# Performance work log

Hardware: AMD Instinct MI355X
Metric: run time of the kernel (lower is better)

Reference implementation:

```python
import jax, jax.numpy as jnp
import numpy as np

B, S, D, F, E, TOPK = 4, 2048, 1024, 4096, 8, 2


def setup_inputs() -> dict:
    key = jax.random.key(0)
    ks = jax.random.split(key, 8)
    sc = 0.02
    return {
        "x": jax.random.normal(ks[0], (B, S, D), dtype=jnp.float32),
        "Wg": jax.random.normal(ks[1], (D, E), dtype=jnp.float32) * sc,
        "bg": jnp.zeros((E,), dtype=jnp.float32),
        "W1": jax.random.normal(ks[2], (E, D, F), dtype=jnp.float32) * sc,
        "b1": jnp.zeros((E, F), dtype=jnp.float32),
        "W2": jax.random.normal(ks[3], (E, F, D), dtype=jnp.float32) * sc,
        "b2": jnp.zeros((E, D), dtype=jnp.float32),
    }


def reference(x, Wg, bg, W1, b1, W2, b2):
    # Router: top-k over gate logits, softmax over the k selected logits.
    logits = jnp.einsum("bsd,de->bse", x, Wg) + bg            # [B,S,E]
    top_vals, top_idx = jax.lax.top_k(logits, TOPK)            # [B,S,K]
    gates = jax.nn.softmax(top_vals, axis=-1)                  # [B,S,K]
    # Combine weights per expert: zero for unselected experts (same math
    # as the original masked gather/scatter loop). [B,S,E]
    comb = jnp.sum(jax.nn.one_hot(top_idx, E, dtype=x.dtype) * gates[..., None], axis=-2)
    xf = x.reshape(-1, D)                                      # [T,D], T=B*S
    cf = comb.reshape(-1, E)                                   # [T,E]
    # Expert FFNs (dropout is identity in eval): relu(x W1 + b1) W2 + b2
    h = jax.nn.relu(jnp.einsum("td,edf->etf", xf, W1) + b1[:, None, :])  # [E,T,F]
    y = jnp.einsum("etf,efd->etd", h, W2) + b2[:, None, :]               # [E,T,D]
    out = jnp.einsum("te,etd->td", cf, y)                                # [T,D]
    return out.reshape(B, S, D)
```

## Files before the change

### kernel.cpp

```cpp
#include <hip/hip_runtime.h>
#include <hip/hip_bf16.h>

#define T_TOK 8192
#define D_DIM 1024
#define F_DIM 4096
#define E_NUM 8
#define BM 128
#define MAX_ROWS (2 * T_TOK + E_NUM * BM)
#define NUM_RB (MAX_ROWS / BM)

typedef __hip_bfloat16 bf16;
using bf16x8  = __attribute__((ext_vector_type(8))) __bf16;
using float4v = __attribute__((ext_vector_type(4))) float;

__device__ inline void gl_lds16(const bf16* g, bf16* l) {
    __builtin_amdgcn_global_load_lds(
        (const __attribute__((address_space(1))) void*)g,
        (__attribute__((address_space(3))) void*)l, 16, 0, 0);
}

#define PH(WAITSTR, CA, CB, DOSTAGE, KST)                                      \
    do {                                                                       \
        asm volatile("s_waitcnt " WAITSTR ::: "memory");                       \
        __builtin_amdgcn_s_barrier();                                          \
        bf16x8 af[4], bfr[4];                                                  \
        _Pragma("unroll")                                                      \
        for (int m_ = 0; m_ < 4; ++m_)                                         \
            af[m_] = *(const bf16x8*)&(CA)[(wrow + m_ * 16 + fr) * 32 + fkk];  \
        _Pragma("unroll")                                                      \
        for (int n_ = 0; n_ < 4; ++n_)                                         \
            bfr[n_] = *(const bf16x8*)&(CB)[(wcol + n_ * 16 + fr) * 32 + fkk]; \
        asm volatile("s_waitcnt lgkmcnt(0)" ::: "memory");                     \
        __builtin_amdgcn_sched_barrier(0);                                     \
        __builtin_amdgcn_s_barrier();                                          \
        if (DOSTAGE) stage(KST, CA, CB);                                       \
        __builtin_amdgcn_s_setprio(1);                                         \
        _Pragma("unroll")                                                      \
        for (int m_ = 0; m_ < 4; ++m_)                                         \
            _Pragma("unroll")                                                  \
            for (int n_ = 0; n_ < 4; ++n_)                                     \
                acc[m_][n_] = __builtin_amdgcn_mfma_f32_16x16x32_bf16(         \
                    af[m_], bfr[n_], acc[m_][n_], 0, 0, 0);                    \
        __builtin_amdgcn_s_setprio(0);                                         \
    } while (0)

__global__ __launch_bounds__(256) void transpose_both(
    const float* __restrict__ W1, bf16* __restrict__ W1t,
    const float* __restrict__ W2, bf16* __restrict__ W2t) {
    __shared__ float tile[64][65];
    const int flat = blockIdx.x;
    const float* s;
    bf16* d;
    int M, N, n0, m0;
    if (flat < 8192) {
        const int e = flat >> 10, rem = flat & 1023;
        M = D_DIM; N = F_DIM;
        n0 = (rem & 63) * 64; m0 = (rem >> 6) * 64;
        s = W1 + (size_t)e * M * N;
        d = W1t + (size_t)e * M * N;
    } else {
        const int f2 = flat - 8192;
        const int e = f2 >> 10, rem = f2 & 1023;
        M = F_DIM; N = D_DIM;
        n0 = (rem & 15) * 64; m0 = (rem >> 4) * 64;
        s = W2 + (size_t)e * M * N;
        d = W2t + (size_t)e * M * N;
    }
    const int tx = threadIdx.x & 15, ty = threadIdx.x >> 4;
#pragma unroll
    for (int i = 0; i < 4; ++i) {
        const int r = ty + i * 16;
        const float4 v = *(const float4*)&s[(size_t)(m0 + r) * N + n0 + tx * 4];
        tile[r][tx * 4 + 0] = v.x;
        tile[r][tx * 4 + 1] = v.y;
        tile[r][tx * 4 + 2] = v.z;
        tile[r][tx * 4 + 3] = v.w;
    }
    __syncthreads();
#pragma unroll
    for (int i = 0; i < 4; ++i) {
        const int nc = ty + i * 16;
        bf16 o[4];
#pragma unroll
        for (int j = 0; j < 4; ++j) o[j] = __float2bfloat16(tile[tx * 4 + j][nc]);
        *(ushort4*)&d[(size_t)(n0 + nc) * M + m0 + tx * 4] = *(const ushort4*)o;
    }
}

__global__ __launch_bounds__(256) void router_xcvt_kernel(
    const float* __restrict__ x, const float* __restrict__ Wg,
    const float* __restrict__ bg, int* __restrict__ top_idx,
    float* __restrict__ top_gate, bf16* __restrict__ xb) {
    const int lane = threadIdx.x & 63;
    const int t = blockIdx.x * 4 + (threadIdx.x >> 6);
    const float* xrow = x + (size_t)t * D_DIM;

    float acc[E_NUM];
#pragma unroll
    for (int e = 0; e < E_NUM; ++e) acc[e] = 0.f;
#pragma unroll
    for (int it = 0; it < D_DIM / 64; ++it) {
        const int d = it * 64 + lane;
        const float xv = xrow[d];
        const float4 w0 = *(const float4*)&Wg[d * 8];
        const float4 w1 = *(const float4*)&Wg[d * 8 + 4];
        acc[0] += xv * w0.x; acc[1] += xv * w0.y;
        acc[2] += xv * w0.z; acc[3] += xv * w0.w;
        acc[4] += xv * w1.x; acc[5] += xv * w1.y;
        acc[6] += xv * w1.z; acc[7] += xv * w1.w;
    }
#pragma unroll
    for (int off = 32; off > 0; off >>= 1) {
#pragma unroll
        for (int e = 0; e < E_NUM; ++e) acc[e] += __shfl_xor(acc[e], off, 64);
    }
    if (lane == 0) {
        float v[E_NUM];
#pragma unroll
        for (int e = 0; e < E_NUM; ++e) v[e] = acc[e] + bg[e];
        int i0 = 0;
#pragma unroll
        for (int e = 1; e < E_NUM; ++e)
            if (v[e] > v[i0]) i0 = e;
        int i1 = -1;
#pragma unroll
        for (int e = 0; e < E_NUM; ++e) {
            if (e == i0) continue;
            if (i1 < 0 || v[e] > v[i1]) i1 = e;
        }
        const float g0 = 1.f / (1.f + expf(v[i1] - v[i0]));
        top_idx[2 * t] = i0;
        top_idx[2 * t + 1] = i1;
        top_gate[2 * t] = g0;
        top_gate[2 * t + 1] = 1.f - g0;
    }
    const float4* xs = (const float4*)(x + (size_t)blockIdx.x * 4 * D_DIM);
    ushort4* xd = (ushort4*)(xb + (size_t)blockIdx.x * 4 * D_DIM);
    for (int i = threadIdx.x; i < D_DIM; i += 256) {
        float4 v = xs[i];
        bf16 tmp[4];
        tmp[0] = __float2bfloat16(v.x);
        tmp[1] = __float2bfloat16(v.y);
        tmp[2] = __float2bfloat16(v.z);
        tmp[3] = __float2bfloat16(v.w);
        xd[i] = *(const ushort4*)tmp;
    }
}

__global__ __launch_bounds__(256) void count_offsets_kernel(
    const int* __restrict__ top_idx, int* __restrict__ offsets) {
    __shared__ int whist[4][E_NUM];
    int cnt[E_NUM];
#pragma unroll
    for (int e = 0; e < E_NUM; ++e) cnt[e] = 0;
    for (int i = threadIdx.x; i < 2 * T_TOK; i += 256) {
        const int idx = top_idx[i];
#pragma unroll
        for (int e = 0; e < E_NUM; ++e) cnt[e] += (idx == e) ? 1 : 0;
    }
#pragma unroll
    for (int off = 32; off > 0; off >>= 1) {
#pragma unroll
        for (int e = 0; e < E_NUM; ++e) cnt[e] += __shfl_xor(cnt[e], off, 64);
    }
    const int lane = threadIdx.x & 63, w = threadIdx.x >> 6;
    if (lane == 0) {
#pragma unroll
        for (int e = 0; e < E_NUM; ++e) whist[w][e] = cnt[e];
    }
    __syncthreads();
    if (threadIdx.x == 0) {
        int o = 0;
#pragma unroll
        for (int e = 0; e < E_NUM; ++e) {
            const int c = whist[0][e] + whist[1][e] + whist[2][e] + whist[3][e];
            offsets[e] = o;
            o += (c + BM - 1) / BM * BM;
        }
        offsets[E_NUM] = o;
    }
}

__global__ __launch_bounds__(256) void scatter_kernel(
    const int* __restrict__ top_idx, const float* __restrict__ top_gate,
    const int* __restrict__ offsets, int* __restrict__ cursors,
    int* __restrict__ tok_list, float* __restrict__ gate_list) {
    __shared__ int lhist[E_NUM];
    __shared__ int lbase[E_NUM];
    if (threadIdx.x < E_NUM) lhist[threadIdx.x] = 0;
    __syncthreads();

    const int t = blockIdx.x * 256 + threadIdx.x;
    int e0 = top_idx[2 * t], e1 = top_idx[2 * t + 1];
    int p0 = atomicAdd(&lhist[e0], 1);
    int p1 = atomicAdd(&lhist[e1], 1);
    __syncthreads();
    if (threadIdx.x < E_NUM)
        lbase[threadIdx.x] = atomicAdd(&cursors[threadIdx.x], lhist[threadIdx.x]);
    __syncthreads();

    const float g0 = top_gate[2 * t], g1 = top_gate[2 * t + 1];
    const int s0 = offsets[e0] + lbase[e0] + p0;
    const int s1 = offsets[e1] + lbase[e1] + p1;
    tok_list[s0] = t;
    gate_list[s0] = g0;
    tok_list[s1] = t;
    gate_list[s1] = g1;
}

__global__ __launch_bounds__(256, 4) void gemm1_kernel(
    const bf16* __restrict__ xb, const bf16* __restrict__ W1t,
    const float* __restrict__ b1, const int* __restrict__ tok_list,
    const int* __restrict__ offsets, bf16* __restrict__ hbuf) {
    __shared__ bf16 As0[BM * 32];
    __shared__ bf16 As1[BM * 32];
    __shared__ bf16 Bs0[BM * 32];
    __shared__ bf16 Bs1[BM * 32];
    __shared__ int toks[BM];

    const int NCB = F_DIM / 128;
    const int per = (NUM_RB * NCB) / 8;
    const int flat = blockIdx.x;
    const int sw = (flat & 7) * per + (flat >> 3);
    const int rb = sw / NCB, cb = sw % NCB;

    const int row0 = rb * BM;
    const int total = offsets[E_NUM];
    if (row0 >= total) return;
    int e = 0;
#pragma unroll
    for (int i = 1; i < E_NUM; ++i) e += (row0 >= offsets[i]) ? 1 : 0;

    const int tid = threadIdx.x;
    if (tid < BM) toks[tid] = tok_list[row0 + tid];
    __syncthreads();

    const int lane = tid & 63;
    const int w = tid >> 6;
    const int f0 = cb * 128;

    const int r0 = w * 16 + (lane >> 2);
    const int r1 = 64 + w * 16 + (lane >> 2);
    const int c16 = (lane & 3) ^ ((lane >> 3) & 3);
    int t0 = toks[r0]; if (t0 < 0) t0 = 0;
    int t1 = toks[r1]; if (t1 < 0) t1 = 0;
    const bf16* aP0 = xb + (size_t)t0 * D_DIM + c16 * 8;
    const bf16* aP1 = xb + (size_t)t1 * D_DIM + c16 * 8;
    const bf16* bP0 = W1t + ((size_t)e * F_DIM + f0 + r0) * D_DIM + c16 * 8;
    const bf16* bP1 = W1t + ((size_t)e * F_DIM + f0 + r1) * D_DIM + c16 * 8;

    const unsigned dO0 = __builtin_amdgcn_readfirstlane(w * 1024);
    const unsigned dO1 = __builtin_amdgcn_readfirstlane(4096 + w * 1024);

    const int wrow = (w >> 1) * 64, wcol = (w & 1) * 64;
    const int fr = lane & 15;
    const int fkk = 8 * ((lane >> 4) ^ ((lane >> 1) & 3));

    float4v acc[4][4];
#pragma unroll
    for (int m = 0; m < 4; ++m)
#pragma unroll
        for (int n = 0; n < 4; ++n)
#pragma unroll
            for (int r = 0; r < 4; ++r) acc[m][n][r] = 0.f;

    auto stage = [&](int kt, bf16* A, bf16* B) {
        const int ko = kt * 32;
        gl_lds16(aP0 + ko, (bf16*)((char*)A + dO0));
        gl_lds16(aP1 + ko, (bf16*)((char*)A + dO1));
        gl_lds16(bP0 + ko, (bf16*)((char*)B + dO0));
        gl_lds16(bP1 + ko, (bf16*)((char*)B + dO1));
    };

    const int NKT = D_DIM / 32;
    stage(0, As0, Bs0);
    stage(1, As1, Bs1);
    for (int kt = 0; kt < NKT - 2; kt += 2) {
        PH("vmcnt(4)", As0, Bs0, true, kt + 2);
        PH("vmcnt(4)", As1, Bs1, true, kt + 3);
    }
    PH("vmcnt(4)", As0, Bs0, false, 0);
    PH("vmcnt(0)", As1, Bs1, false, 0);

#pragma unroll
    for (int n = 0; n < 4; ++n) {
        const int gcol = f0 + wcol + n * 16 + fr;
        const float bias = b1[e * F_DIM + gcol];
#pragma unroll
        for (int m = 0; m < 4; ++m) {
#pragma unroll
            for (int r = 0; r < 4; ++r) {
                const int grow = row0 + wrow + m * 16 + (lane >> 4) * 4 + r;
                float v = acc[m][n][r] + bias;
                v = fmaxf(v, 0.f);
                hbuf[(size_t)grow * F_DIM + gcol] = __float2bfloat16(v);
            }
        }
    }
}

__global__ __launch_bounds__(256, 4) void gemm2_kernel(
    const bf16* __restrict__ hbuf, const bf16* __restrict__ W2t,
    const float* __restrict__ b2, const int* __restrict__ tok_list,
    const float* __restrict__ gate_list, const int* __restrict__ offsets,
    float* __restrict__ out) {
    __shared__ bf16 As0[BM * 32];
    __shared__ bf16 As1[BM * 32];
    __shared__ bf16 Bs0[BM * 32];
    __shared__ bf16 Bs1[BM * 32];
    __shared__ int toks[BM];
    __shared__ float gates_s[BM];

    const int NCB = D_DIM / 128;
    const int per = (NUM_RB * NCB) / 8;
    const int flat = blockIdx.x;
    const int sw = (flat & 7) * per + (flat >> 3);
    const int rb = sw / NCB, cb = sw % NCB;

    const int row0 = rb * BM;
    const int total = offsets[E_NUM];
    if (row0 >= total) return;
    int e = 0;
#pragma unroll
    for (int i = 1; i < E_NUM; ++i) e += (row0 >= offsets[i]) ? 1 : 0;

    const int tid = threadIdx.x;
    if (tid < BM) {
        int t = tok_list[row0 + tid];
        toks[tid] = t;
        gates_s[tid] = (t >= 0) ? gate_list[row0 + tid] : 0.f;
    }
    __syncthreads();

    const int lane = tid & 63;
    const int w = tid >> 6;
    const int d0 = cb * 128;

    const int r0 = w * 16 + (lane >> 2);
    const int r1 = 64 + w * 16 + (lane >> 2);
    const int c16 = (lane & 3) ^ ((lane >> 3) & 3);
    const bf16* aP0 = hbuf + (size_t)(row0 + r0) * F_DIM + c16 * 8;
    const bf16* aP1 = hbuf + (size_t)(row0 + r1) * F_DIM + c16 * 8;
    const bf16* bP0 = W2t + ((size_t)e * D_DIM + d0 + r0) * F_DIM + c16 * 8;
    const bf16* bP1 = W2t + ((size_t)e * D_DIM + d0 + r1) * F_DIM + c16 * 8;

    const unsigned dO0 = __builtin_amdgcn_readfirstlane(w * 1024);
    const unsigned dO1 = __builtin_amdgcn_readfirstlane(4096 + w * 1024);

    const int wrow = (w >> 1) * 64, wcol = (w & 1) * 64;
    const int fr = lane & 15;
    const int fkk = 8 * ((lane >> 4) ^ ((lane >> 1) & 3));

    float4v acc[4][4];
#pragma unroll
    for (int m = 0; m < 4; ++m)
#pragma unroll
        for (int n = 0; n < 4; ++n)
#pragma unroll
            for (int r = 0; r < 4; ++r) acc[m][n][r] = 0.f;

    auto stage = [&](int kt, bf16* A, bf16* B) {
        const int ko = kt * 32;
        gl_lds16(aP0 + ko, (bf16*)((char*)A + dO0));
        gl_lds16(aP1 + ko, (bf16*)((char*)A + dO1));
        gl_lds16(bP0 + ko, (bf16*)((char*)B + dO0));
        gl_lds16(bP1 + ko, (bf16*)((char*)B + dO1));
    };

    const int NKT = F_DIM / 32;
    stage(0, As0, Bs0);
    stage(1, As1, Bs1);
    for (int kt = 0; kt < NKT - 2; kt += 2) {
        PH("vmcnt(4)", As0, Bs0, true, kt + 2);
        PH("vmcnt(4)", As1, Bs1, true, kt + 3);
    }
    PH("vmcnt(4)", As0, Bs0, false, 0);
    PH("vmcnt(0)", As1, Bs1, false, 0);

#pragma unroll
    for (int n = 0; n < 4; ++n) {
        const int gcol = d0 + wcol + n * 16 + fr;
        const float bias = b2[e * D_DIM + gcol];
#pragma unroll
        for (int m = 0; m < 4; ++m) {
#pragma unroll
            for (int r = 0; r < 4; ++r) {
                const int lrow = wrow + m * 16 + (lane >> 4) * 4 + r;
                const int t = toks[lrow];
                if (t >= 0) {
                    const float v = (acc[m][n][r] + bias) * gates_s[lrow];
                    atomicAdd(&out[(size_t)t * D_DIM + gcol], v);
                }
            }
        }
    }
}

extern "C" void kernel_launch(void* const* d_in, const int* in_sizes, int n_in,
                              void* d_out, int out_size, void* d_ws, size_t ws_size,
                              hipStream_t stream) {
    const float* x = (const float*)d_in[0];
    const float* Wg = (const float*)d_in[1];
    const float* bg = (const float*)d_in[2];
    const float* W1 = (const float*)d_in[3];
    const float* b1 = (const float*)d_in[4];
    const float* W2 = (const float*)d_in[5];
    const float* b2 = (const float*)d_in[6];
    float* out = (float*)d_out;

    char* ws = (char*)d_ws;
    int* cursors = (int*)(ws + 32);
    int* offsets = (int*)(ws + 64);
    int* top_idx = (int*)(ws + 256);
    float* top_gate = (float*)(ws + 256 + 65536);
    int* tok_list = (int*)(ws + 256 + 2 * 65536);
    float* gate_list = (float*)(ws + 256 + 2 * 65536 + 69632);
    size_t off = 256 + 2 * 65536 + 2 * 69632;
    bf16* xb = (bf16*)(ws + off);
    off += (size_t)T_TOK * D_DIM * 2;
    bf16* W1t = (bf16*)(ws + off);
    off += (size_t)E_NUM * D_DIM * F_DIM * 2;
    bf16* W2t = (bf16*)(ws + off);
    off += (size_t)E_NUM * D_DIM * F_DIM * 2;
    bf16* hbuf = (bf16*)(ws + off);

    hipMemsetAsync(d_out, 0, (size_t)T_TOK * D_DIM * sizeof(float), stream);
    hipMemsetAsync(ws, 0, 64, stream);
    hipMemsetAsync(tok_list, 0xFF, (size_t)MAX_ROWS * 4, stream);

    transpose_both<<<16384, 256, 0, stream>>>(W1, W1t, W2, W2t);
    router_xcvt_kernel<<<T_TOK / 4, 256, 0, stream>>>(x, Wg, bg, top_idx, top_gate, xb);
    count_offsets_kernel<<<1, 256, 0, stream>>>(top_idx, offsets);
    scatter_kernel<<<T_TOK / 256, 256, 0, stream>>>(top_idx, top_gate, offsets, cursors,
                                                    tok_list, gate_list);
    gemm1_kernel<<<NUM_RB * (F_DIM / 128), 256, 0, stream>>>(xb, W1t, b1, tok_list,
                                                             offsets, hbuf);
    gemm2_kernel<<<NUM_RB * (D_DIM / 128), 256, 0, stream>>>(hbuf, W2t, b2, tok_list,
                                                             gate_list, offsets, out);
}
```

Baseline: 583.5 us.

## Replace atomic scatter with per-slot output buffer and reduction; fuse transposes into other kernels

gemm2 now writes gated expert outputs to a per-slot buffer instead of atomically adding into the output. A new reduce kernel sums each token's two slots using slot indices recorded by the scatter kernel, which also removes the output memset. The W1 transpose is merged into the router launch and the W2 transpose into the gemm1 launch as extra blocks, so they can overlap with other work. The change adds a large intermediate write and read, and reuses the xb/W1t workspace region for that buffer.

```diff
diff --git a/kernel.cpp b/kernel.cpp
--- a/kernel.cpp
+++ b/kernel.cpp
@@ -8,6 +8,7 @@
 #define BM 128
 #define MAX_ROWS (2 * T_TOK + E_NUM * BM)
 #define NUM_RB (MAX_ROWS / BM)
+#define G1_BLOCKS (NUM_RB * (F_DIM / 128))
 
 typedef __hip_bfloat16 bf16;
 using bf16x8  = __attribute__((ext_vector_type(8))) __bf16;
@@ -44,28 +45,8 @@
         __builtin_amdgcn_s_setprio(0);                                         \
     } while (0)
 
-__global__ __launch_bounds__(256) void transpose_both(
-    const float* __restrict__ W1, bf16* __restrict__ W1t,
-    const float* __restrict__ W2, bf16* __restrict__ W2t) {
-    __shared__ float tile[64][65];
-    const int flat = blockIdx.x;
-    const float* s;
-    bf16* d;
-    int M, N, n0, m0;
-    if (flat < 8192) {
-        const int e = flat >> 10, rem = flat & 1023;
-        M = D_DIM; N = F_DIM;
-        n0 = (rem & 63) * 64; m0 = (rem >> 6) * 64;
-        s = W1 + (size_t)e * M * N;
-        d = W1t + (size_t)e * M * N;
-    } else {
-        const int f2 = flat - 8192;
-        const int e = f2 >> 10, rem = f2 & 1023;
-        M = F_DIM; N = D_DIM;
-        n0 = (rem & 15) * 64; m0 = (rem >> 4) * 64;
-        s = W2 + (size_t)e * M * N;
-        d = W2t + (size_t)e * M * N;
-    }
+__device__ inline void transpose_tile(const float* s, bf16* d, int N, int M,
+                                      int n0, int m0, float (*tile)[65]) {
     const int tx = threadIdx.x & 15, ty = threadIdx.x >> 4;
 #pragma unroll
     for (int i = 0; i < 4; ++i) {
@@ -87,12 +68,24 @@
     }
 }
 
-__global__ __launch_bounds__(256) void router_xcvt_kernel(
+__global__ __launch_bounds__(256) void prepA_kernel(
+    const float* __restrict__ W1, bf16* __restrict__ W1t,
     const float* __restrict__ x, const float* __restrict__ Wg,
     const float* __restrict__ bg, int* __restrict__ top_idx,
     float* __restrict__ top_gate, bf16* __restrict__ xb) {
+    __shared__ alignas(16) char pool[16640];
+    const int bid = blockIdx.x;
+    if (bid < 8192) {
+        const int e = bid >> 10, rem = bid & 1023;
+        const int n0 = (rem & 63) * 64, m0 = (rem >> 6) * 64;
+        transpose_tile(W1 + (size_t)e * D_DIM * F_DIM,
+                       W1t + (size_t)e * D_DIM * F_DIM,
+                       F_DIM, D_DIM, n0, m0, (float(*)[65])pool);
+        return;
+    }
+    const int rbid = bid - 8192;
     const int lane = threadIdx.x & 63;
-    const int t = blockIdx.x * 4 + (threadIdx.x >> 6);
+    const int t = rbid * 4 + (threadIdx.x >> 6);
     const float* xrow = x + (size_t)t * D_DIM;
 
     float acc[E_NUM];
@@ -134,8 +127,8 @@
         top_gate[2 * t] = g0;
         top_gate[2 * t + 1] = 1.f - g0;
     }
-    const float4* xs = (const float4*)(x + (size_t)blockIdx.x * 4 * D_DIM);
-    ushort4* xd = (ushort4*)(xb + (size_t)blockIdx.x * 4 * D_DIM);
+    const float4* xs = (const float4*)(x + (size_t)rbid * 4 * D_DIM);
+    ushort4* xd = (ushort4*)(xb + (size_t)rbid * 4 * D_DIM);
     for (int i = threadIdx.x; i < D_DIM; i += 256) {
         float4 v = xs[i];
         bf16 tmp[4];
@@ -184,7 +177,8 @@
 __global__ __launch_bounds__(256) void scatter_kernel(
     const int* __restrict__ top_idx, const float* __restrict__ top_gate,
     const int* __restrict__ offsets, int* __restrict__ cursors,
-    int* __restrict__ tok_list, float* __restrict__ gate_list) {
+    int* __restrict__ tok_list, float* __restrict__ gate_list,
+    int* __restrict__ tok_slots) {
     __shared__ int lhist[E_NUM];
     __shared__ int lbase[E_NUM];
     if (threadIdx.x < E_NUM) lhist[threadIdx.x] = 0;
@@ -206,17 +200,30 @@
     gate_list[s0] = g0;
     tok_list[s1] = t;
     gate_list[s1] = g1;
-}
-
-__global__ __launch_bounds__(256, 4) void gemm1_kernel(
+    tok_slots[2 * t] = s0;
+    tok_slots[2 * t + 1] = s1;
+}
+
+__global__ __launch_bounds__(256, 4) void gemm1_w2t_kernel(
     const bf16* __restrict__ xb, const bf16* __restrict__ W1t,
     const float* __restrict__ b1, const int* __restrict__ tok_list,
-    const int* __restrict__ offsets, bf16* __restrict__ hbuf) {
-    __shared__ bf16 As0[BM * 32];
-    __shared__ bf16 As1[BM * 32];
-    __shared__ bf16 Bs0[BM * 32];
-    __shared__ bf16 Bs1[BM * 32];
-    __shared__ int toks[BM];
+    const int* __restrict__ offsets, bf16* __restrict__ hbuf,
+    const float* __restrict__ W2, bf16* __restrict__ W2t) {
+    __shared__ alignas(16) char pool[33280];
+    if (blockIdx.x >= G1_BLOCKS) {
+        const int f2 = blockIdx.x - G1_BLOCKS;
+        const int e = f2 >> 10, rem = f2 & 1023;
+        const int n0 = (rem & 15) * 64, m0 = (rem >> 4) * 64;
+        transpose_tile(W2 + (size_t)e * D_DIM * F_DIM,
+                       W2t + (size_t)e * D_DIM * F_DIM,
+                       D_DIM, F_DIM, n0, m0, (float(*)[65])pool);
+        return;
+    }
+    bf16* As0 = (bf16*)pool;
+    bf16* As1 = (bf16*)(pool + 8192);
+    bf16* Bs0 = (bf16*)(pool + 16384);
+    bf16* Bs1 = (bf16*)(pool + 24576);
+    int* toks = (int*)(pool + 32768);
 
     const int NCB = F_DIM / 128;
     const int per = (NUM_RB * NCB) / 8;
@@ -303,12 +310,11 @@
     const bf16* __restrict__ hbuf, const bf16* __restrict__ W2t,
     const float* __restrict__ b2, const int* __restrict__ tok_list,
     const float* __restrict__ gate_list, const int* __restrict__ offsets,
-    float* __restrict__ out) {
+    float* __restrict__ y) {
     __shared__ bf16 As0[BM * 32];
     __shared__ bf16 As1[BM * 32];
     __shared__ bf16 Bs0[BM * 32];
     __shared__ bf16 Bs1[BM * 32];
-    __shared__ int toks[BM];
     __shared__ float gates_s[BM];
 
     const int NCB = D_DIM / 128;
@@ -327,7 +333,6 @@
     const int tid = threadIdx.x;
     if (tid < BM) {
         int t = tok_list[row0 + tid];
-        toks[tid] = t;
         gates_s[tid] = (t >= 0) ? gate_list[row0 + tid] : 0.f;
     }
     __syncthreads();
@@ -386,14 +391,24 @@
 #pragma unroll
             for (int r = 0; r < 4; ++r) {
                 const int lrow = wrow + m * 16 + (lane >> 4) * 4 + r;
-                const int t = toks[lrow];
-                if (t >= 0) {
-                    const float v = (acc[m][n][r] + bias) * gates_s[lrow];
-                    atomicAdd(&out[(size_t)t * D_DIM + gcol], v);
-                }
+                const float v = (acc[m][n][r] + bias) * gates_s[lrow];
+                y[(size_t)(row0 + lrow) * D_DIM + gcol] = v;
             }
         }
     }
+}
+
+__global__ __launch_bounds__(256) void reduce_kernel(
+    const float* __restrict__ y, const int* __restrict__ tok_slots,
+    float* __restrict__ out) {
+    const int t = blockIdx.x;
+    const int s0 = tok_slots[2 * t], s1 = tok_slots[2 * t + 1];
+    const float4* y0 = (const float4*)(y + (size_t)s0 * D_DIM);
+    const float4* y1 = (const float4*)(y + (size_t)s1 * D_DIM);
+    float4* o = (float4*)(out + (size_t)t * D_DIM);
+    const int i = threadIdx.x;
+    const float4 a = y0[i], b = y1[i];
+    o[i] = make_float4(a.x + b.x, a.y + b.y, a.z + b.z, a.w + b.w);
 }
 
 extern "C" void kernel_launch(void* const* d_in, const int* in_sizes, int n_in,
@@ -415,8 +430,10 @@
     float* top_gate = (float*)(ws + 256 + 65536);
     int* tok_list = (int*)(ws + 256 + 2 * 65536);
     float* gate_list = (float*)(ws + 256 + 2 * 65536 + 69632);
-    size_t off = 256 + 2 * 65536 + 2 * 69632;
+    int* tok_slots = (int*)(ws + 270592);
+    size_t off = 270592 + 65536;
     bf16* xb = (bf16*)(ws + off);
+    float* y = (float*)(ws + off);
     off += (size_t)T_TOK * D_DIM * 2;
     bf16* W1t = (bf16*)(ws + off);
     off += (size_t)E_NUM * D_DIM * F_DIM * 2;
@@ -424,17 +441,17 @@
     off += (size_t)E_NUM * D_DIM * F_DIM * 2;
     bf16* hbuf = (bf16*)(ws + off);
 
-    hipMemsetAsync(d_out, 0, (size_t)T_TOK * D_DIM * sizeof(float), stream);
     hipMemsetAsync(ws, 0, 64, stream);
     hipMemsetAsync(tok_list, 0xFF, (size_t)MAX_ROWS * 4, stream);
 
-    transpose_both<<<16384, 256, 0, stream>>>(W1, W1t, W2, W2t);
-    router_xcvt_kernel<<<T_TOK / 4, 256, 0, stream>>>(x, Wg, bg, top_idx, top_gate, xb);
+    prepA_kernel<<<8192 + T_TOK / 4, 256, 0, stream>>>(W1, W1t, x, Wg, bg,
+                                                       top_idx, top_gate, xb);
     count_offsets_kernel<<<1, 256, 0, stream>>>(top_idx, offsets);
     scatter_kernel<<<T_TOK / 256, 256, 0, stream>>>(top_idx, top_gate, offsets, cursors,
-                                                    tok_list, gate_list);
-    gemm1_kernel<<<NUM_RB * (F_DIM / 128), 256, 0, stream>>>(xb, W1t, b1, tok_list,
-                                                             offsets, hbuf);
+                                                    tok_list, gate_list, tok_slots);
+    gemm1_w2t_kernel<<<G1_BLOCKS + 8192, 256, 0, stream>>>(xb, W1t, b1, tok_list,
+                                                           offsets, hbuf, W2, W2t);
     gemm2_kernel<<<NUM_RB * (D_DIM / 128), 256, 0, stream>>>(hbuf, W2t, b2, tok_list,
-                                                             gate_list, offsets, out);
-}
+                                                             gate_list, offsets, y);
+    reduce_kernel<<<T_TOK, 256, 0, stream>>>(y, tok_slots, out);
+}
```

After: 528.4 us. 1.1x faster.
